# Performance work log

Measured on AMD Instinct MI355X. Metric: run time of the kernel, lower is better.

The kernel has to match this reference:

```python
import jax, jax.numpy as jnp
import numpy as np

B, L, E, D = 4, 2048, 512, 128


def setup_inputs() -> dict:
    key = jax.random.key(0)
    k1, k2 = jax.random.split(key)
    emb_sentences = jax.random.normal(k1, (B, L, E), dtype=jnp.float32)
    # torch nn.Linear weight layout: [out_dim, in_dim]
    W = jax.random.normal(k2, (D, E), dtype=jnp.float32) * (1.0 / np.sqrt(E))
    return {"emb_sentences": emb_sentences, "W": W}


def reference(emb_sentences, W):
    # dep_embeddings = Linear(emb) with no bias: [B, L, D]
    dep = jnp.einsum('ble,de->bld', emb_sentences, W)
    # All-pairs squared Euclidean distances without the O(L^2 * D)
    # broadcast intermediate: ||xi - xj||^2 = ||xi||^2 + ||xj||^2 - 2 xi.xj
    sq = jnp.sum(dep * dep, axis=-1)                 # [B, L]
    gram = jnp.einsum('bid,bjd->bij', dep, dep)      # [B, L, L]
    distances = sq[:, :, None] + sq[:, None, :] - 2.0 * gram
    return dep, distances
```

## Files before the change

kernel.cpp:

```cpp
#include <hip/hip_runtime.h>
#include <hip/hip_bf16.h>


typedef __attribute__((ext_vector_type(8))) short  short8;
typedef __attribute__((ext_vector_type(4))) float  floatx4;
typedef __attribute__((ext_vector_type(4))) unsigned short ushortx4;

#define B_  4
#define L_  2048
#define E_  512
#define D_  128
#define M_  (B_*L_)

__device__ __forceinline__ unsigned short f2bfu(float x) {
    __hip_bfloat16 h = __float2bfloat16(x);
    union { __hip_bfloat16 h; unsigned short u; } c; c.h = h; return c.u;
}
__device__ __forceinline__ float bfu2f(unsigned short u) {
    union { unsigned u32; float f; } c; c.u32 = ((unsigned)u) << 16; return c.f;
}
__device__ __forceinline__ short8 cvt8(const float* p) {
    float4 x = *reinterpret_cast<const float4*>(p);
    float4 y = *reinterpret_cast<const float4*>(p + 4);
    short8 t;
    t[0] = (short)f2bfu(x.x); t[1] = (short)f2bfu(x.y);
    t[2] = (short)f2bfu(x.z); t[3] = (short)f2bfu(x.w);
    t[4] = (short)f2bfu(y.x); t[5] = (short)f2bfu(y.y);
    t[6] = (short)f2bfu(y.z); t[7] = (short)f2bfu(y.w);
    return t;
}

__global__ __launch_bounds__(256)
void kP1(const float* __restrict__ emb, const float* __restrict__ W,
         float* __restrict__ dep_out, unsigned short* __restrict__ dep_b16,
         float* __restrict__ sq)
{
    __shared__ float pws[16][4];
    const int tid  = threadIdx.x;
    const int lane = tid & 63, wave = tid >> 6;
    const int l15 = lane & 15, lg = lane >> 4;
    const long m0 = (long)blockIdx.x * 16;

    floatx4 acc[2] = { (floatx4){0.f,0.f,0.f,0.f}, (floatx4){0.f,0.f,0.f,0.f} };
    const float* ar = emb + (m0 + l15) * E_;
    const float* w0 = W + (wave * 32 + l15) * E_;
    const float* w1 = W + (wave * 32 + 16 + l15) * E_;

    #pragma unroll
    for (int k0 = 0; k0 < E_; k0 += 32) {
        const int kc = k0 + lg * 8;
        short8 bfm = cvt8(ar + kc);
        short8 af0 = cvt8(w0 + kc);
        short8 af1 = cvt8(w1 + kc);
        acc[0] = __builtin_amdgcn_mfma_f32_16x16x32_bf16(af0, bfm, acc[0], 0, 0, 0);
        acc[1] = __builtin_amdgcn_mfma_f32_16x16x32_bf16(af1, bfm, acc[1], 0, 0, 0);
    }

    const long m = m0 + l15;
    float p = 0.f;
    #pragma unroll
    for (int ni = 0; ni < 2; ++ni) {
        const int dbase = wave * 32 + ni * 16 + lg * 4;
        floatx4  v;
        ushortx4 u;
        #pragma unroll
        for (int j = 0; j < 4; ++j) {
            v[j] = acc[ni][j];
            u[j] = f2bfu(v[j]);
            float vb = bfu2f(u[j]);
            p += vb * vb;
        }
        *reinterpret_cast<floatx4*>(dep_out + m * D_ + dbase)  = v;
        *reinterpret_cast<ushortx4*>(dep_b16 + m * D_ + dbase) = u;
    }
    p += __shfl_xor(p, 16);
    p += __shfl_xor(p, 32);
    if (lane < 16) pws[lane][wave] = p;
    __syncthreads();
    if (tid < 16)
        sq[m0 + tid] = pws[tid][0] + pws[tid][1] + pws[tid][2] + pws[tid][3];
}

__global__ __launch_bounds__(256)
void kP2(const unsigned short* __restrict__ dep_b16, const float* __restrict__ sq,
         float* __restrict__ dist)
{
    __shared__ __align__(16) unsigned short Is[128][136];
    __shared__ __align__(16) unsigned short Js[128][136];

    const int tid  = threadIdx.x;
    const int lane = tid & 63;
    const int wave = tid >> 6;
    const int wr = wave >> 1, wc = wave & 1;
    const int l15 = lane & 15, lg = lane >> 4;
    const int b  = blockIdx.z;
    const int i0 = blockIdx.y * 128;
    const int j0 = blockIdx.x * 128;
    const unsigned short* depb = dep_b16 + (long)b * L_ * D_;

    #pragma unroll
    for (int jj = 0; jj < 8; ++jj) {
        int chunk = tid + 256 * jj;
        int row = chunk >> 4, c8 = chunk & 15;
        *reinterpret_cast<short8*>(&Is[row][c8 * 8]) =
            *reinterpret_cast<const short8*>(depb + (long)(i0 + row) * D_ + c8 * 8);
        *reinterpret_cast<short8*>(&Js[row][c8 * 8]) =
            *reinterpret_cast<const short8*>(depb + (long)(j0 + row) * D_ + c8 * 8);
    }
    __syncthreads();

    floatx4 acc[4][4];
    #pragma unroll
    for (int i = 0; i < 4; ++i)
        #pragma unroll
        for (int j = 0; j < 4; ++j)
            acc[i][j] = (floatx4){0.f, 0.f, 0.f, 0.f};

    #pragma unroll
    for (int kk = 0; kk < 4; ++kk) {
        short8 af[4], bf[4];
        #pragma unroll
        for (int mi = 0; mi < 4; ++mi)
            af[mi] = *reinterpret_cast<const short8*>(&Is[wr * 64 + mi * 16 + l15][kk * 32 + lg * 8]);
        #pragma unroll
        for (int ni = 0; ni < 4; ++ni)
            bf[ni] = *reinterpret_cast<const short8*>(&Js[wc * 64 + ni * 16 + l15][kk * 32 + lg * 8]);
        #pragma unroll
        for (int mi = 0; mi < 4; ++mi)
            #pragma unroll
            for (int ni = 0; ni < 4; ++ni)
                acc[mi][ni] = __builtin_amdgcn_mfma_f32_16x16x32_bf16(
                    bf[ni], af[mi], acc[mi][ni], 0, 0, 0);
    }

    const float* sqb = sq + b * L_;
    float sri[4];
    #pragma unroll
    for (int mi = 0; mi < 4; ++mi)
        sri[mi] = sqb[i0 + wr * 64 + mi * 16 + l15];
    floatx4 sqj[4];
    #pragma unroll
    for (int ni = 0; ni < 4; ++ni)
        sqj[ni] = *reinterpret_cast<const floatx4*>(sqb + j0 + wc * 64 + ni * 16 + lg * 4);

    float* db = dist + (long)b * L_ * L_;
    #pragma unroll
    for (int mi = 0; mi < 4; ++mi) {
        const long i = i0 + wr * 64 + mi * 16 + l15;
        #pragma unroll
        for (int ni = 0; ni < 4; ++ni) {
            const int jb = j0 + wc * 64 + ni * 16 + lg * 4;
            floatx4 v;
            #pragma unroll
            for (int jj = 0; jj < 4; ++jj)
                v[jj] = sri[mi] + sqj[ni][jj] - 2.0f * acc[mi][ni][jj];
            *reinterpret_cast<floatx4*>(db + i * L_ + jb) = v;
        }
    }
}

extern "C" void kernel_launch(void* const* d_in, const int* in_sizes, int n_in,
                              void* d_out, int out_size, void* d_ws, size_t ws_size,
                              hipStream_t stream)
{
    const float* emb = (const float*)d_in[0];
    const float* W   = (const float*)d_in[1];

    float* dep_out = (float*)d_out;
    float* dist    = dep_out + (size_t)M_ * D_;

    unsigned short* dep_b16 = (unsigned short*)d_ws;
    float* sq = (float*)((char*)d_ws + (size_t)M_ * D_ * sizeof(unsigned short));

    hipLaunchKernelGGL(kP1, dim3(M_ / 16), dim3(256), 0, stream,
                       emb, W, dep_out, dep_b16, sq);
    hipLaunchKernelGGL(kP2, dim3(L_ / 128, L_ / 128, B_), dim3(256), 0, stream,
                       dep_b16, sq, dist);
}
```

Before: 48.06 us.

## Pre-convert W to bf16, stream I-tile from global, interleave MFMA with stores

Adds a small kernel that converts W to bf16 once per call, so kP1 loads bf16 weights directly instead of converting fp32 for every block. In kP2 the I tile no longer goes through LDS. Each wave loads its A fragments from global with double buffering, and computes one 16-row slab of MFMAs at a time, writing that slab's distances before the next. The aim is to overlap the large distance stores with compute and to cut LDS size and register pressure (launch bounds now allow 4 blocks). A swizzled 1D grid also changes the order in which blocks are scheduled. The cost is an extra kernel launch and uncoalesced global fragment loads for I.

New measurement: 49.21 us. 2.4% more time.

```diff
diff --git a/kernel.cpp b/kernel.cpp
--- a/kernel.cpp
+++ b/kernel.cpp
@@ -31,7 +31,17 @@
 }
 
 __global__ __launch_bounds__(256)
-void kP1(const float* __restrict__ emb, const float* __restrict__ W,
+void kW(const float* __restrict__ W, unsigned short* __restrict__ Wb)
+{
+    int i = (blockIdx.x * 256 + threadIdx.x) * 4;
+    float4 v = *reinterpret_cast<const float4*>(W + i);
+    ushort4 u;
+    u.x = f2bfu(v.x); u.y = f2bfu(v.y); u.z = f2bfu(v.z); u.w = f2bfu(v.w);
+    *reinterpret_cast<ushort4*>(Wb + i) = u;
+}
+
+__global__ __launch_bounds__(256)
+void kP1(const float* __restrict__ emb, const unsigned short* __restrict__ Wb,
          float* __restrict__ dep_out, unsigned short* __restrict__ dep_b16,
          float* __restrict__ sq)
 {
@@ -43,15 +53,15 @@
 
     floatx4 acc[2] = { (floatx4){0.f,0.f,0.f,0.f}, (floatx4){0.f,0.f,0.f,0.f} };
     const float* ar = emb + (m0 + l15) * E_;
-    const float* w0 = W + (wave * 32 + l15) * E_;
-    const float* w1 = W + (wave * 32 + 16 + l15) * E_;
+    const unsigned short* w0 = Wb + (wave * 32 + l15) * E_;
+    const unsigned short* w1 = Wb + (wave * 32 + 16 + l15) * E_;
 
     #pragma unroll
     for (int k0 = 0; k0 < E_; k0 += 32) {
         const int kc = k0 + lg * 8;
         short8 bfm = cvt8(ar + kc);
-        short8 af0 = cvt8(w0 + kc);
-        short8 af1 = cvt8(w1 + kc);
+        short8 af0 = *reinterpret_cast<const short8*>(w0 + kc);
+        short8 af1 = *reinterpret_cast<const short8*>(w1 + kc);
         acc[0] = __builtin_amdgcn_mfma_f32_16x16x32_bf16(af0, bfm, acc[0], 0, 0, 0);
         acc[1] = __builtin_amdgcn_mfma_f32_16x16x32_bf16(af1, bfm, acc[1], 0, 0, 0);
     }
@@ -81,11 +91,10 @@
         sq[m0 + tid] = pws[tid][0] + pws[tid][1] + pws[tid][2] + pws[tid][3];
 }
 
-__global__ __launch_bounds__(256)
+__global__ __launch_bounds__(256, 4)
 void kP2(const unsigned short* __restrict__ dep_b16, const float* __restrict__ sq,
          float* __restrict__ dist)
 {
-    __shared__ __align__(16) unsigned short Is[128][136];
     __shared__ __align__(16) unsigned short Js[128][136];
 
     const int tid  = threadIdx.x;
@@ -93,45 +102,27 @@
     const int wave = tid >> 6;
     const int wr = wave >> 1, wc = wave & 1;
     const int l15 = lane & 15, lg = lane >> 4;
-    const int b  = blockIdx.z;
-    const int i0 = blockIdx.y * 128;
-    const int j0 = blockIdx.x * 128;
+
+    const int swz = (blockIdx.x & 7) * 128 + (blockIdx.x >> 3);
+    const int b  = swz >> 8;
+    const int i0 = ((swz >> 4) & 15) * 128;
+    const int j0 = (swz & 15) * 128;
     const unsigned short* depb = dep_b16 + (long)b * L_ * D_;
 
     #pragma unroll
     for (int jj = 0; jj < 8; ++jj) {
         int chunk = tid + 256 * jj;
         int row = chunk >> 4, c8 = chunk & 15;
-        *reinterpret_cast<short8*>(&Is[row][c8 * 8]) =
-            *reinterpret_cast<const short8*>(depb + (long)(i0 + row) * D_ + c8 * 8);
         *reinterpret_cast<short8*>(&Js[row][c8 * 8]) =
             *reinterpret_cast<const short8*>(depb + (long)(j0 + row) * D_ + c8 * 8);
     }
-    __syncthreads();
 
-    floatx4 acc[4][4];
+    const unsigned short* ibase = depb + (long)(i0 + wr * 64 + l15) * D_ + lg * 8;
+
+    short8 af[2][4];
     #pragma unroll
-    for (int i = 0; i < 4; ++i)
-        #pragma unroll
-        for (int j = 0; j < 4; ++j)
-            acc[i][j] = (floatx4){0.f, 0.f, 0.f, 0.f};
-
-    #pragma unroll
-    for (int kk = 0; kk < 4; ++kk) {
-        short8 af[4], bf[4];
-        #pragma unroll
-        for (int mi = 0; mi < 4; ++mi)
-            af[mi] = *reinterpret_cast<const short8*>(&Is[wr * 64 + mi * 16 + l15][kk * 32 + lg * 8]);
-        #pragma unroll
-        for (int ni = 0; ni < 4; ++ni)
-            bf[ni] = *reinterpret_cast<const short8*>(&Js[wc * 64 + ni * 16 + l15][kk * 32 + lg * 8]);
-        #pragma unroll
-        for (int mi = 0; mi < 4; ++mi)
-            #pragma unroll
-            for (int ni = 0; ni < 4; ++ni)
-                acc[mi][ni] = __builtin_amdgcn_mfma_f32_16x16x32_bf16(
-                    bf[ni], af[mi], acc[mi][ni], 0, 0, 0);
-    }
+    for (int kk = 0; kk < 4; ++kk)
+        af[0][kk] = *reinterpret_cast<const short8*>(ibase + kk * 32);
 
     const float* sqb = sq + b * L_;
     float sri[4];
@@ -143,9 +134,31 @@
     for (int ni = 0; ni < 4; ++ni)
         sqj[ni] = *reinterpret_cast<const floatx4*>(sqb + j0 + wc * 64 + ni * 16 + lg * 4);
 
+    __syncthreads();
+
     float* db = dist + (long)b * L_ * L_;
     #pragma unroll
     for (int mi = 0; mi < 4; ++mi) {
+        if (mi < 3) {
+            #pragma unroll
+            for (int kk = 0; kk < 4; ++kk)
+                af[(mi + 1) & 1][kk] = *reinterpret_cast<const short8*>(
+                    ibase + (long)(mi + 1) * 16 * D_ + kk * 32);
+        }
+        floatx4 acc[4];
+        #pragma unroll
+        for (int ni = 0; ni < 4; ++ni)
+            acc[ni] = (floatx4){0.f, 0.f, 0.f, 0.f};
+        #pragma unroll
+        for (int ni = 0; ni < 4; ++ni) {
+            #pragma unroll
+            for (int kk = 0; kk < 4; ++kk) {
+                short8 bf = *reinterpret_cast<const short8*>(
+                    &Js[wc * 64 + ni * 16 + l15][kk * 32 + lg * 8]);
+                acc[ni] = __builtin_amdgcn_mfma_f32_16x16x32_bf16(
+                    bf, af[mi & 1][kk], acc[ni], 0, 0, 0);
+            }
+        }
         const long i = i0 + wr * 64 + mi * 16 + l15;
         #pragma unroll
         for (int ni = 0; ni < 4; ++ni) {
@@ -153,7 +166,7 @@
             floatx4 v;
             #pragma unroll
             for (int jj = 0; jj < 4; ++jj)
-                v[jj] = sri[mi] + sqj[ni][jj] - 2.0f * acc[mi][ni][jj];
+                v[jj] = sri[mi] + sqj[ni][jj] - 2.0f * acc[ni][jj];
             *reinterpret_cast<floatx4*>(db + i * L_ + jb) = v;
         }
     }
@@ -171,9 +184,11 @@
 
     unsigned short* dep_b16 = (unsigned short*)d_ws;
     float* sq = (float*)((char*)d_ws + (size_t)M_ * D_ * sizeof(unsigned short));
+    unsigned short* Wb = (unsigned short*)((char*)sq + (size_t)M_ * sizeof(float));
 
+    hipLaunchKernelGGL(kW,  dim3((D_ * E_) / (256 * 4)), dim3(256), 0, stream, W, Wb);
     hipLaunchKernelGGL(kP1, dim3(M_ / 16), dim3(256), 0, stream,
-                       emb, W, dep_out, dep_b16, sq);
-    hipLaunchKernelGGL(kP2, dim3(L_ / 128, L_ / 128, B_), dim3(256), 0, stream,
+                       emb, Wb, dep_out, dep_b16, sq);
+    hipLaunchKernelGGL(kP2, dim3(16 * 16 * B_), dim3(256), 0, stream,
                        dep_b16, sq, dist);
 }
```
